# Optimization experiments

Hardware: AMD Instinct MI355X
Metric: run time of the kernel (lower is better)

Reference implementation:

```python
import jax, jax.numpy as jnp
import numpy as np

B, C, H, W, OC, K = 8, 256, 120, 120, 256, 3


def setup_inputs() -> dict:
    key = jax.random.key(0)
    ks = jax.random.split(key, 6)
    x = jax.random.normal(ks[0], (B, C, H, W), jnp.float32)
    y = jax.random.normal(ks[1], (B, C, H, W), jnp.float32)
    # generate_kernel: 1x1 conv in_yC -> in_xC (weight stored as (out, in))
    gen_w = jax.random.normal(ks[2], (C, C), jnp.float32) * (1.0 / np.sqrt(C))
    gen_b = jax.random.normal(ks[3], (C,), jnp.float32) * 0.01
    # fuse: 3x3 conv in_xC -> out_C, padding 1
    fuse_w = jax.random.normal(ks[4], (OC, C, 3, 3), jnp.float32) * (1.0 / np.sqrt(C * 9))
    fuse_b = jax.random.normal(ks[5], (OC,), jnp.float32) * 0.01
    return {"x": x, "y": y, "gen_w": gen_w, "gen_b": gen_b,
            "fuse_w": fuse_w, "fuse_b": fuse_b}


def reference(x, y, gen_w, gen_b, fuse_w, fuse_b):
    b, c, h, w = x.shape
    # AdaptiveAvgPool2d(K): H,W divisible by K -> uniform average pooling
    yp = y.reshape(b, c, K, h // K, K, w // K).mean(axis=(3, 5))  # (B,C,K,K)
    # 1x1 conv to generate per-sample per-channel kernels
    kernel = jnp.einsum('oc,bcij->boij', gen_w, yp) + gen_b[None, :, None, None]
    # dynamic depthwise conv: groups = B*C, padding 1 (cross-correlation, as torch)
    xg = x.reshape(1, b * c, h, w)
    kg = kernel.reshape(b * c, 1, K, K)
    dn = jax.lax.conv_dimension_numbers(xg.shape, kg.shape, ('NCHW', 'OIHW', 'NCHW'))
    out = jax.lax.conv_general_dilated(
        xg, kg, window_strides=(1, 1), padding=((1, 1), (1, 1)),
        dimension_numbers=dn, feature_group_count=b * c)
    out = out.reshape(b, c, h, w)
    # fuse: dense 3x3 conv C -> OC, padding 1, with bias
    dn2 = jax.lax.conv_dimension_numbers(out.shape, fuse_w.shape, ('NCHW', 'OIHW', 'NCHW'))
    res = jax.lax.conv_general_dilated(
        out, fuse_w, window_strides=(1, 1), padding=((1, 1), (1, 1)),
        dimension_numbers=dn2)
    return res + fuse_b[None, :, None, None]
```

## Files before the change

### kernel.cpp

```cpp
#include <hip/hip_runtime.h>
#include <hip/hip_bf16.h>
#include <stdint.h>

#define TB 8
#define TC 256
#define TH 120
#define TW 120
#define THW 14400
#define TOC 256
#define PH 122
#define PW 122

typedef short bf16x8 __attribute__((ext_vector_type(8)));
typedef float f32x4 __attribute__((ext_vector_type(4)));

#define OUTP_BYTES ((size_t)TB * PH * PW * TC * 2)
#define YP_OFF     OUTP_BYTES
#define DK_OFF     (YP_OFF + (size_t)TB * TC * 9 * 4)
#define WP_OFF     (DK_OFF + (size_t)TB * TC * 9 * 4)

__global__ __launch_bounds__(128) void pool_prep_kernel(
        const float* __restrict__ y, float* __restrict__ yp,
        const float* __restrict__ fuse_w, __hip_bfloat16* __restrict__ Wp,
        char* __restrict__ outP) {
    int blk = blockIdx.x;
    int t = threadIdx.x;
    __shared__ float red[128][3];
    if (blk < 2048) {
        int bc = blk;
        const float4* img = (const float4*)(y + (size_t)bc * THW);
        int cq = t & 31;
        int rsub = t >> 5;
        bool act = cq < 30;
        float a0 = 0.f, a1 = 0.f, a2 = 0.f;
        if (act) {
            #pragma unroll
            for (int k = 0; k < 30; ++k) {
                int row = k * 4 + rsub;
                float4 v = img[row * 30 + cq];
                float s = (v.x + v.y) + (v.z + v.w);
                if (k < 10) a0 += s; else if (k < 20) a1 += s; else a2 += s;
            }
        }
        red[t][0] = a0; red[t][1] = a1; red[t][2] = a2;
        __syncthreads();
        if (t < 9) {
            int bh = t / 3, bw = t - bh * 3;
            float a = 0.f;
            #pragma unroll
            for (int g = 0; g < 4; ++g)
                for (int q = 0; q < 10; ++q)
                    a += red[g * 32 + bw * 10 + q][bh];
            yp[bc * 9 + t] = a * (1.f / 1600.f);
        }
    } else if (blk < 3016) {
        int i = (blk - 2048) * 128 + t;
        int pos_idx = i >> 5, part = i & 31;
        int b = pos_idx / 484; int k = pos_idx - b * 484;
        int h, w;
        if (k < 122)      { h = 0;   w = k; }
        else if (k < 244) { h = 121; w = k - 122; }
        else { int m = k - 244; h = 1 + (m >> 1); w = (m & 1) ? 121 : 0; }
        size_t pos = ((size_t)b * PH + h) * PW + w;
        uint4 z; z.x = 0u; z.y = 0u; z.z = 0u; z.w = 0u;
        *(uint4*)(outP + pos * 512 + part * 16) = z;
    } else {
        int i = (blk - 3016) * 128 + t;
        int ij = i >> 16;
        int oc = (i >> 8) & 255;
        int c  = i & 255;
        Wp[i] = __float2bfloat16(fuse_w[(oc * 256 + c) * 9 + ij]);
    }
}

__global__ __launch_bounds__(256) void gen_kernel(const float* __restrict__ yp,
        const float* __restrict__ gen_w, const float* __restrict__ gen_b,
        float* __restrict__ dk) {
    int blk = blockIdx.x;
    int b = blk >> 3, ocg = blk & 7;
    int t = threadIdx.x;
    int ocl = t & 31, cseg = t >> 5;
    int oc = ocg * 32 + ocl;
    __shared__ float yps[TC * 9];
    for (int i = t; i < TC * 9; i += 256) yps[i] = yp[b * TC * 9 + i];
    __syncthreads();
    float acc[9];
    #pragma unroll
    for (int j = 0; j < 9; ++j) acc[j] = 0.f;
    const float* wrow = gen_w + (size_t)oc * TC + cseg * 32;
    for (int c = 0; c < 32; ++c) {
        float w = wrow[c];
        const float* yrow = &yps[(cseg * 32 + c) * 9];
        #pragma unroll
        for (int j = 0; j < 9; ++j) acc[j] += w * yrow[j];
    }
    __shared__ float red[8][32][9];
    #pragma unroll
    for (int j = 0; j < 9; ++j) red[cseg][ocl][j] = acc[j];
    __syncthreads();
    for (int st = 4; st > 0; st >>= 1) {
        if (cseg < st) {
            #pragma unroll
            for (int j = 0; j < 9; ++j) red[cseg][ocl][j] += red[cseg + st][ocl][j];
        }
        __syncthreads();
    }
    if (cseg == 0) {
        float bias = gen_b[oc];
        #pragma unroll
        for (int j = 0; j < 9; ++j)
            dk[((size_t)b * TC + oc) * 9 + j] = red[0][ocl][j] + bias;
    }
}

__global__ __launch_bounds__(1024) void dw_kernel(const float* __restrict__ x,
        const float* __restrict__ dk, __hip_bfloat16* __restrict__ outP) {
    int bid = blockIdx.x;
    int hs = bid & 7;
    int cc = (bid >> 3) & 7;
    int b  = bid >> 6;
    int t = threadIdx.x;
    int c  = t >> 5;
    int wq = t & 31;
    bool active = wq < 30;
    int w0 = wq * 4;
    int cg = cc * 32 + c;
    const float* xp = x + (size_t)(b * TC + cg) * THW;
    const float* dkp = dk + (size_t)(b * TC + cg) * 9;
    float k0[3], k1[3], k2[3];
    #pragma unroll
    for (int j = 0; j < 3; ++j) { k0[j] = dkp[j]; k1[j] = dkp[3 + j]; k2[j] = dkp[6 + j]; }

    __shared__ __align__(16) __hip_bfloat16 stage[2][2][32][124];

    int h0 = hs * 15;
    float A[6], B[6], C[6];
    auto loadrow = [&](int hh, float* V) {
        if (hh < 0 || hh >= TH) {
            #pragma unroll
            for (int j = 0; j < 6; ++j) V[j] = 0.f;
            return;
        }
        const float* row = xp + hh * TW;
        float4 v = *(const float4*)(row + w0);
        V[1] = v.x; V[2] = v.y; V[3] = v.z; V[4] = v.w;
        V[0] = (wq > 0)  ? row[w0 - 1] : 0.f;
        V[5] = (wq < 29) ? row[w0 + 4] : 0.f;
    };
    auto comp = [&](int r, int par, int sub) {
        if (!active) return;
        loadrow(h0 + r + 1, C);
        ushort4 pk;
        #pragma unroll
        for (int i = 0; i < 4; ++i) {
            float o = A[i] * k0[0] + A[i + 1] * k0[1] + A[i + 2] * k0[2]
                    + B[i] * k1[0] + B[i + 1] * k1[1] + B[i + 2] * k1[2]
                    + C[i] * k2[0] + C[i + 1] * k2[1] + C[i + 2] * k2[2];
            __hip_bfloat16 hb = __float2bfloat16(o);
            ushort u = *(ushort*)&hb;
            if (i == 0) pk.x = u; else if (i == 1) pk.y = u;
            else if (i == 2) pk.z = u; else pk.w = u;
        }
        *(ushort4*)&stage[par][sub][c][w0] = pk;
        #pragma unroll
        for (int j = 0; j < 6; ++j) { A[j] = B[j]; B[j] = C[j]; }
    };
    auto flushrow = [&](int r, int par, int sub, int tt) {
        int w = tt >> 2, part = tt & 3;
        ushort vals[8];
        #pragma unroll
        for (int j = 0; j < 8; ++j) vals[j] = *(const ushort*)&stage[par][sub][part * 8 + j][w];
        uint4 o;
        o.x = (uint)vals[0] | ((uint)vals[1] << 16);
        o.y = (uint)vals[2] | ((uint)vals[3] << 16);
        o.z = (uint)vals[4] | ((uint)vals[5] << 16);
        o.w = (uint)vals[6] | ((uint)vals[7] << 16);
        size_t pos = ((size_t)b * PH + (h0 + r + 1)) * PW + (w + 1);
        *(uint4*)((char*)outP + pos * 512 + cc * 64 + part * 16) = o;
    };

    if (active) { loadrow(h0 - 1, A); loadrow(h0, B); }
    comp(0, 0, 0); comp(1, 0, 1);
    __syncthreads();
    #pragma unroll 1
    for (int p = 1; p < 8; ++p) {
        int r0 = 2 * p;
        comp(r0, p & 1, 0);
        if (r0 + 1 < 15) comp(r0 + 1, p & 1, 1);
        if (t < 960) {
            int fr = t >= 480 ? 1 : 0;
            int tt = t - fr * 480;
            flushrow(2 * (p - 1) + fr, (p - 1) & 1, fr, tt);
        }
        __syncthreads();
    }
    if (t < 480) flushrow(14, 1, 0, t);
}

typedef const __attribute__((address_space(1))) char* gas_t;
typedef __attribute__((address_space(3))) char* las_t;
__device__ __forceinline__ void gload16(const char* g, char* l) {
    __builtin_amdgcn_global_load_lds((gas_t)g, (las_t)l, 16, 0, 0);
}

__global__ __launch_bounds__(256, 2) void gemm_kernel(
        const __hip_bfloat16* __restrict__ outP,
        const __hip_bfloat16* __restrict__ Wp,
        const float* __restrict__ fuse_b,
        float* __restrict__ res) {
    __shared__ __align__(16) char lds[2][32768];
    const int t = threadIdx.x;
    const int lane = t & 63;
    const int wv = t >> 6;
    const int wo = wv >> 1;
    const int wm = wv & 1;

    const int bid0 = blockIdx.x;
    const int logical = (bid0 & 7) * 225 + (bid0 >> 3);
    const int bn = logical & 1;
    const int bm = logical >> 1;

    const char* gI = (const char*)outP;
    const char* gW = (const char*)Wp;

    const int rbp = (((lane & 7) ^ (lane >> 3)) << 4);
    int srcI[4], srcW[4];
    #pragma unroll
    for (int q = 0; q < 4; ++q) {
        int p = (q * 4 + wv) * 8 + (lane >> 3);
        int m = bm * 128 + p;
        int b = m / THW; int r = m - b * THW;
        int h = r / TW;  int w = r - h * TW;
        srcI[q] = (((b * PH + h) * PW + w) << 9) + rbp;
        srcW[q] = ((bn * 128 + p) << 9) + rbp;
    }
    const int segBase = wv * 1024;

    int aWb[4], aWs[4], aIb[4], aIs[4];
    #pragma unroll
    for (int i = 0; i < 4; ++i) {
        int rw = wo * 64 + i * 16 + (lane & 15);
        aWb[i] = rw * 128; aWs[i] = (rw & 7) << 4;
        int ri = wm * 64 + i * 16 + (lane & 15);
        aIb[i] = ri * 128; aIs[i] = (ri & 7) << 4;
    }
    const int klo = (lane >> 4) << 4;

    f32x4 acc[4][4];
    #pragma unroll
    for (int i = 0; i < 4; ++i) {
        #pragma unroll
        for (int j = 0; j < 4; ++j) {
            f32x4 z = {0.f, 0.f, 0.f, 0.f};
            acc[i][j] = z;
        }
    }

    auto step_offs = [&](int s, int& offI, int& offW) {
        int ij = s >> 2;
        int c0b = (s & 3) << 7;
        int di = ij / 3, dj = ij - (ij / 3) * 3;
        offI = ((di * PW + dj) << 9) + c0b;
        offW = (ij << 17) + c0b;
    };
    auto STAGE = [&](int buf, int s) {
        int offI, offW; step_offs(s, offI, offW);
        char* LI = &lds[buf][0];
        char* LW = &lds[buf][16384];
        #pragma unroll
        for (int q = 0; q < 4; ++q) {
            gload16(gI + srcI[q] + offI, LI + segBase + q * 4096);
            gload16(gW + srcW[q] + offW, LW + segBase + q * 4096);
        }
    };
    auto COMPUTE = [&](int buf) {
        const char* LI = &lds[buf][0];
        const char* LW = &lds[buf][16384];
        #pragma unroll
        for (int kk = 0; kk < 2; ++kk) {
            int ck = kk * 64 + klo;
            bf16x8 wf[4], iff[4];
            #pragma unroll
            for (int i = 0; i < 4; ++i)
                wf[i] = *(const bf16x8*)(LW + aWb[i] + (ck ^ aWs[i]));
            #pragma unroll
            for (int i = 0; i < 4; ++i)
                iff[i] = *(const bf16x8*)(LI + aIb[i] + (ck ^ aIs[i]));
            __builtin_amdgcn_s_setprio(1);
            #pragma unroll
            for (int o = 0; o < 4; ++o) {
                #pragma unroll
                for (int mi = 0; mi < 4; ++mi)
                    acc[o][mi] = __builtin_amdgcn_mfma_f32_16x16x32_bf16(
                        wf[o], iff[mi], acc[o][mi], 0, 0, 0);
            }
            __builtin_amdgcn_s_setprio(0);
        }
    };

    STAGE(0, 0);
    #pragma unroll 1
    for (int s = 0; s < 35; ++s) {
        int cur = s & 1;
        STAGE(cur ^ 1, s + 1);
        asm volatile("s_waitcnt vmcnt(8)" ::: "memory");
        __builtin_amdgcn_s_barrier();
        asm volatile("" ::: "memory");
        COMPUTE(cur);
        asm volatile("" ::: "memory");
        __builtin_amdgcn_s_barrier();
        asm volatile("" ::: "memory");
    }
    asm volatile("s_waitcnt vmcnt(0)" ::: "memory");
    __builtin_amdgcn_s_barrier();
    asm volatile("" ::: "memory");
    COMPUTE(1);

    int baseM[4];
    #pragma unroll
    for (int mt = 0; mt < 4; ++mt) {
        int m = bm * 128 + wm * 64 + mt * 16 + (lane & 15);
        int b = m / THW; int r = m - b * THW;
        baseM[mt] = b * (TOC * THW) + r;
    }
    const int ocb0 = bn * 128 + wo * 64 + ((lane >> 4) << 2);
    float bias[4][4];
    #pragma unroll
    for (int o = 0; o < 4; ++o) {
        #pragma unroll
        for (int g = 0; g < 4; ++g)
            bias[o][g] = fuse_b[ocb0 + o * 16 + g];
    }
    #pragma unroll
    for (int o = 0; o < 4; ++o) {
        #pragma unroll
        for (int mt = 0; mt < 4; ++mt) {
            #pragma unroll
            for (int g = 0; g < 4; ++g)
                res[baseM[mt] + (ocb0 + o * 16 + g) * THW] = acc[o][mt][g] + bias[o][g];
        }
    }
}

extern "C" void kernel_launch(void* const* d_in, const int* in_sizes, int n_in,
                              void* d_out, int out_size, void* d_ws, size_t ws_size,
                              hipStream_t stream) {
    const float* x      = (const float*)d_in[0];
    const float* y      = (const float*)d_in[1];
    const float* gen_w  = (const float*)d_in[2];
    const float* gen_b  = (const float*)d_in[3];
    const float* fuse_w = (const float*)d_in[4];
    const float* fuse_b = (const float*)d_in[5];
    float* out = (float*)d_out;
    char* ws = (char*)d_ws;

    __hip_bfloat16* outP = (__hip_bfloat16*)(ws);
    float* yp = (float*)(ws + YP_OFF);
    float* dk = (float*)(ws + DK_OFF);
    __hip_bfloat16* Wp = (__hip_bfloat16*)(ws + WP_OFF);

    pool_prep_kernel<<<7624, 128, 0, stream>>>(y, yp, fuse_w, Wp, (char*)outP);
    gen_kernel<<<64, 256, 0, stream>>>(yp, gen_w, gen_b, dk);
    dw_kernel<<<512, 1024, 0, stream>>>(x, dk, outP);
    gemm_kernel<<<1800, 256, 0, stream>>>(outP, Wp, fuse_b, out);
}
```

Baseline: 216.8 us.

## Load GEMM weight fragments directly into registers, halving LDS to raise occupancy

The weight (B) operand of the implicit-GEMM conv is no longer staged through LDS. Each lane now loads its MFMA fragments straight from global memory into double-buffered registers. Only the input tile remains in LDS, which halves shared memory per block and lets launch bounds target 3 blocks per CU. In exchange, register pressure rises and duplicated global weight loads across waves (served from cache rather than shared) could limit the gain.

```diff
diff --git a/kernel.cpp b/kernel.cpp
--- a/kernel.cpp
+++ b/kernel.cpp
@@ -203,12 +203,12 @@
     __builtin_amdgcn_global_load_lds((gas_t)g, (las_t)l, 16, 0, 0);
 }
 
-__global__ __launch_bounds__(256, 2) void gemm_kernel(
+__global__ __launch_bounds__(256, 3) void gemm_kernel(
         const __hip_bfloat16* __restrict__ outP,
         const __hip_bfloat16* __restrict__ Wp,
         const float* __restrict__ fuse_b,
         float* __restrict__ res) {
-    __shared__ __align__(16) char lds[2][32768];
+    __shared__ __align__(16) char lds[2][16384];
     const int t = threadIdx.x;
     const int lane = t & 63;
     const int wv = t >> 6;
@@ -224,7 +224,7 @@
     const char* gW = (const char*)Wp;
 
     const int rbp = (((lane & 7) ^ (lane >> 3)) << 4);
-    int srcI[4], srcW[4];
+    int srcI[4];
     #pragma unroll
     for (int q = 0; q < 4; ++q) {
         int p = (q * 4 + wv) * 8 + (lane >> 3);
@@ -232,19 +232,21 @@
         int b = m / THW; int r = m - b * THW;
         int h = r / TW;  int w = r - h * TW;
         srcI[q] = (((b * PH + h) * PW + w) << 9) + rbp;
-        srcW[q] = ((bn * 128 + p) << 9) + rbp;
     }
     const int segBase = wv * 1024;
 
-    int aWb[4], aWs[4], aIb[4], aIs[4];
+    int aIb[4], aIs[4];
     #pragma unroll
     for (int i = 0; i < 4; ++i) {
-        int rw = wo * 64 + i * 16 + (lane & 15);
-        aWb[i] = rw * 128; aWs[i] = (rw & 7) << 4;
         int ri = wm * 64 + i * 16 + (lane & 15);
         aIb[i] = ri * 128; aIs[i] = (ri & 7) << 4;
     }
     const int klo = (lane >> 4) << 4;
+
+    int srcB[4];
+    #pragma unroll
+    for (int i = 0; i < 4; ++i)
+        srcB[i] = ((bn * 128 + wo * 64 + i * 16 + (lane & 15)) << 9) + klo;
 
     f32x4 acc[4][4];
     #pragma unroll
@@ -256,33 +258,35 @@
         }
     }
 
-    auto step_offs = [&](int s, int& offI, int& offW) {
+    auto offI_of = [&](int s) {
         int ij = s >> 2;
-        int c0b = (s & 3) << 7;
-        int di = ij / 3, dj = ij - (ij / 3) * 3;
-        offI = ((di * PW + dj) << 9) + c0b;
-        offW = (ij << 17) + c0b;
-    };
-    auto STAGE = [&](int buf, int s) {
-        int offI, offW; step_offs(s, offI, offW);
+        int di = ij / 3, dj = ij - di * 3;
+        return ((di * PW + dj) << 9) + ((s & 3) << 7);
+    };
+    auto offW_of = [&](int s) {
+        return ((s >> 2) << 17) + ((s & 3) << 7);
+    };
+    auto STAGE_A = [&](int buf, int s) {
+        int offI = offI_of(s);
         char* LI = &lds[buf][0];
-        char* LW = &lds[buf][16384];
-        #pragma unroll
-        for (int q = 0; q < 4; ++q) {
+        #pragma unroll
+        for (int q = 0; q < 4; ++q)
             gload16(gI + srcI[q] + offI, LI + segBase + q * 4096);
-            gload16(gW + srcW[q] + offW, LW + segBase + q * 4096);
-        }
-    };
-    auto COMPUTE = [&](int buf) {
+    };
+    auto LOADB = [&](bf16x8* dst, int s) {
+        int offW = offW_of(s);
+        #pragma unroll
+        for (int i = 0; i < 4; ++i) {
+            dst[i * 2 + 0] = *(const bf16x8*)(gW + srcB[i] + offW);
+            dst[i * 2 + 1] = *(const bf16x8*)(gW + srcB[i] + offW + 64);
+        }
+    };
+    auto COMPUTE = [&](int buf, const bf16x8* bfr) {
         const char* LI = &lds[buf][0];
-        const char* LW = &lds[buf][16384];
         #pragma unroll
         for (int kk = 0; kk < 2; ++kk) {
             int ck = kk * 64 + klo;
-            bf16x8 wf[4], iff[4];
-            #pragma unroll
-            for (int i = 0; i < 4; ++i)
-                wf[i] = *(const bf16x8*)(LW + aWb[i] + (ck ^ aWs[i]));
+            bf16x8 iff[4];
             #pragma unroll
             for (int i = 0; i < 4; ++i)
                 iff[i] = *(const bf16x8*)(LI + aIb[i] + (ck ^ aIs[i]));
@@ -292,29 +296,42 @@
                 #pragma unroll
                 for (int mi = 0; mi < 4; ++mi)
                     acc[o][mi] = __builtin_amdgcn_mfma_f32_16x16x32_bf16(
-                        wf[o], iff[mi], acc[o][mi], 0, 0, 0);
+                        bfr[o * 2 + kk], iff[mi], acc[o][mi], 0, 0, 0);
             }
             __builtin_amdgcn_s_setprio(0);
         }
     };
 
-    STAGE(0, 0);
+    bf16x8 b0[8], b1[8];
+    STAGE_A(0, 0); LOADB(b0, 0);
     #pragma unroll 1
-    for (int s = 0; s < 35; ++s) {
-        int cur = s & 1;
-        STAGE(cur ^ 1, s + 1);
-        asm volatile("s_waitcnt vmcnt(8)" ::: "memory");
+    for (int s2 = 0; s2 < 18; ++s2) {
+        int s = 2 * s2;
+        if (s + 1 < 36) {
+            STAGE_A(1, s + 1); LOADB(b1, s + 1);
+            asm volatile("s_waitcnt vmcnt(12)" ::: "memory");
+        } else {
+            asm volatile("s_waitcnt vmcnt(0)" ::: "memory");
+        }
         __builtin_amdgcn_s_barrier();
         asm volatile("" ::: "memory");
-        COMPUTE(cur);
+        COMPUTE(0, b0);
         asm volatile("" ::: "memory");
         __builtin_amdgcn_s_barrier();
         asm volatile("" ::: "memory");
-    }
-    asm volatile("s_waitcnt vmcnt(0)" ::: "memory");
-    __builtin_amdgcn_s_barrier();
-    asm volatile("" ::: "memory");
-    COMPUTE(1);
+        if (s + 2 < 36) {
+            STAGE_A(0, s + 2); LOADB(b0, s + 2);
+            asm volatile("s_waitcnt vmcnt(12)" ::: "memory");
+        } else {
+            asm volatile("s_waitcnt vmcnt(0)" ::: "memory");
+        }
+        __builtin_amdgcn_s_barrier();
+        asm volatile("" ::: "memory");
+        COMPUTE(1, b1);
+        asm volatile("" ::: "memory");
+        __builtin_amdgcn_s_barrier();
+        asm volatile("" ::: "memory");
+    }
 
     int baseM[4];
     #pragma unroll
```

Result: slower. 541.9 us (+149.9%).
